# Optimization experiments

Hardware: AMD Instinct MI355X
Metric: run time of the kernel (lower is better)

Reference implementation:

```python
import jax, jax.numpy as jnp
import numpy as np

N_NODES = 100000
N_EDGES = 1600000
IN_FEAT = 128
HIDDEN = 64
OUT_FEAT = 32


def gcn_conv(x, src, dst, W, b, num_nodes):
    """PyG GCNConv: add self-loops, symmetric deg^-1/2 normalization,
    linear transform, scatter-sum aggregation at destination nodes."""
    loops = jnp.arange(num_nodes, dtype=src.dtype)
    s = jnp.concatenate([src, loops])  # [E+N]
    d = jnp.concatenate([dst, loops])  # [E+N]
    deg = jax.ops.segment_sum(jnp.ones_like(d, dtype=x.dtype), d,
                              num_segments=num_nodes)  # in-degree incl. self-loop
    dinv = jnp.where(deg > 0, jax.lax.rsqrt(deg), 0.0)
    norm = dinv[s] * dinv[d]                       # [E+N]
    h = x @ W.T                                    # [N, out] dense GEMM first (PyG order)
    msg = h[s] * norm[:, None]                     # gather + scale, [E+N, out]
    out = jax.ops.segment_sum(msg, d, num_segments=num_nodes)
    return out + b


def setup_inputs() -> dict:
    key = jax.random.key(0)
    k1, k2, k3, k4, k5, k6, k7 = jax.random.split(key, 7)
    x = jax.random.normal(k1, (N_NODES, IN_FEAT), dtype=jnp.float32)
    edge_index = jax.random.randint(k2, (2, N_EDGES), 0, N_NODES, dtype=jnp.int64)
    # Glorot-ish init for linear weights (PyG Linear), zeros bias
    W1 = jax.random.normal(k3, (HIDDEN, IN_FEAT), dtype=jnp.float32) * (1.0 / np.sqrt(IN_FEAT))
    b1 = jnp.zeros((HIDDEN,), dtype=jnp.float32)
    W2 = jax.random.normal(k4, (OUT_FEAT, HIDDEN), dtype=jnp.float32) * (1.0 / np.sqrt(HIDDEN))
    b2 = jnp.zeros((OUT_FEAT,), dtype=jnp.float32)
    return {"x": x, "edge_index": edge_index, "W1": W1, "b1": b1, "W2": W2, "b2": b2}


def reference(x, edge_index, W1, b1, W2, b2):
    src, dst = edge_index[0], edge_index[1]
    h = gcn_conv(x, src, dst, W1, b1, N_NODES)
    h = jax.nn.relu(h)
    # dropout is identity in eval mode (training=False)
    out = gcn_conv(h, src, dst, W2, b2, N_NODES)
    return out
```

## Files before the change

### kernel.cpp

```cpp
#include <hip/hip_runtime.h>
#include <hip/hip_bf16.h>

#define N_NODES 100000
#define N_EDGES 1600000
#define IN_FEAT 128
#define HIDDEN 64
#define OUT_FEAT 32
#define CAP 64
#define NP 100352
#define PS 68
#define PW 36
#define NBINS 256
#define BIN_NODES 391
#define BIN_CAP 8192
#define EB 4096
#define NBB 391

__device__ __forceinline__ float b2f(unsigned short v) {
    union { unsigned int u; float f; } x;
    x.u = ((unsigned int)v) << 16;
    return x.f;
}
__device__ __forceinline__ unsigned short f2b(float f) {
    union { float f; unsigned int u; } x;
    x.f = f;
    unsigned int r = x.u + 0x7FFFu + ((x.u >> 16) & 1u);
    return (unsigned short)(r >> 16);
}


__global__ __launch_bounds__(256) void k_fused0(const int* __restrict__ src,
                                                const int* __restrict__ dst,
                                                int* __restrict__ binc,
                                                int* __restrict__ ebuf,
                                                const float* __restrict__ x,
                                                const float* __restrict__ W,
                                                unsigned short* __restrict__ u,
                                                int n_edges, int n_nodes) {
    __shared__ float wt[IN_FEAT * HIDDEN];
    int t = threadIdx.x;

    if (blockIdx.x < NBB) {
        int* hist  = (int*)wt;
        int* sbase = (int*)wt + 256;
        hist[t] = 0;
        __syncthreads();

        int estart = blockIdx.x * EB + t * 16;
        int rec[16], bn[16], rk[16];
#pragma unroll
        for (int r = 0; r < 4; ++r) {
            int e = estart + 4 * r;
            if (e + 3 < n_edges) {
                int4 d4 = *(const int4*)(dst + e);
                int4 s4 = *(const int4*)(src + e);
                int dd[4] = {d4.x, d4.y, d4.z, d4.w};
                int ss[4] = {s4.x, s4.y, s4.z, s4.w};
#pragma unroll
                for (int c = 0; c < 4; ++c) {
                    int b = dd[c] / BIN_NODES;
                    bn[4 * r + c] = b;
                    rec[4 * r + c] = ss[c] | ((dd[c] - b * BIN_NODES) << 17);
                }
            } else {
#pragma unroll
                for (int c = 0; c < 4; ++c) {
                    int ee = e + c;
                    bool ok = ee < n_edges;
                    int dd = ok ? dst[ee] : 0;
                    int ss = ok ? src[ee] : 0;
                    int b = dd / BIN_NODES;
                    bn[4 * r + c] = ok ? b : -1;
                    rec[4 * r + c] = ss | ((dd - b * BIN_NODES) << 17);
                }
            }
        }
#pragma unroll
        for (int r = 0; r < 16; ++r)
            rk[r] = (bn[r] >= 0) ? atomicAdd(&hist[bn[r]], 1) : 0;
        __syncthreads();
        sbase[t] = (hist[t] > 0) ? atomicAdd(&binc[t], hist[t]) : 0;
        __syncthreads();
#pragma unroll
        for (int r = 0; r < 16; ++r) {
            if (bn[r] >= 0) {
                int pos = sbase[bn[r]] + rk[r];
                if (pos < BIN_CAP)
                    ebuf[(size_t)bn[r] * BIN_CAP + pos] = rec[r];
            }
        }
        return;
    }

    int bid = blockIdx.x - NBB;
    {
        int k4 = t & 31;
        int f0 = t >> 5;
#pragma unroll
        for (int r = 0; r < 8; ++r) {
            int f = f0 + 8 * r;
            float4 wv = *(const float4*)(W + (size_t)f * IN_FEAT + 4 * k4);
            int g = (f >> 2) ^ (k4 & 15);
            int bse = 4 * g + (f & 3);
            wt[(4 * k4 + 0) * HIDDEN + bse] = wv.x;
            wt[(4 * k4 + 1) * HIDDEN + bse] = wv.y;
            wt[(4 * k4 + 2) * HIDDEN + bse] = wv.z;
            wt[(4 * k4 + 3) * HIDDEN + bse] = wv.w;
        }
    }
    __syncthreads();

    int fi = t & 15;
    int ng = t >> 4;
    int node0 = bid * 64 + 4 * ng;

    const float4* xr[4];
#pragma unroll
    for (int m = 0; m < 4; ++m) {
        int nm = node0 + m;
        if (nm > n_nodes - 1) nm = n_nodes - 1;
        xr[m] = (const float4*)(x + (size_t)nm * IN_FEAT);
    }

    float4 acc[4];
#pragma unroll
    for (int m = 0; m < 4; ++m) acc[m] = make_float4(0.f, 0.f, 0.f, 0.f);

#pragma unroll 8
    for (int k4 = 0; k4 < IN_FEAT / 4; ++k4) {
        float4 xv0 = xr[0][k4];
        float4 xv1 = xr[1][k4];
        float4 xv2 = xr[2][k4];
        float4 xv3 = xr[3][k4];
        const float* wp = wt + (4 * k4) * HIDDEN + 4 * (fi ^ (k4 & 15));
        float4 wv0 = *(const float4*)(wp);
        float4 wv1 = *(const float4*)(wp + HIDDEN);
        float4 wv2 = *(const float4*)(wp + 2 * HIDDEN);
        float4 wv3 = *(const float4*)(wp + 3 * HIDDEN);
#define FMA4(A, XV)                                                        \
        A.x += XV.x * wv0.x + XV.y * wv1.x + XV.z * wv2.x + XV.w * wv3.x;  \
        A.y += XV.x * wv0.y + XV.y * wv1.y + XV.z * wv2.y + XV.w * wv3.y;  \
        A.z += XV.x * wv0.z + XV.y * wv1.z + XV.z * wv2.z + XV.w * wv3.z;  \
        A.w += XV.x * wv0.w + XV.y * wv1.w + XV.z * wv2.w + XV.w * wv3.w;
        FMA4(acc[0], xv0)
        FMA4(acc[1], xv1)
        FMA4(acc[2], xv2)
        FMA4(acc[3], xv3)
#undef FMA4
    }

#pragma unroll
    for (int m = 0; m < 4; ++m) {
        int node = node0 + m;
        if (node < n_nodes) {
            ushort4 o;
            o.x = f2b(acc[m].x); o.y = f2b(acc[m].y);
            o.z = f2b(acc[m].z); o.w = f2b(acc[m].w);
            *(ushort4*)(u + (size_t)node * HIDDEN + 4 * fi) = o;
        }
    }
}


__global__ __launch_bounds__(256) void k_binB(const int* __restrict__ binc,
                                              const int* __restrict__ ebuf,
                                              int* __restrict__ csr,
                                              int* __restrict__ deg,
                                              unsigned short* __restrict__ u,
                                              unsigned short* __restrict__ h2,
                                              int n_nodes) {
    __shared__ int lcur[BIN_NODES];
    int t = threadIdx.x;
    int b = blockIdx.x;

    for (int i = t; i < BIN_NODES; i += 256) lcur[i] = 0;
    __syncthreads();

    int cnt = binc[b];
    if (cnt > BIN_CAP) cnt = BIN_CAP;
    const int* eb = ebuf + (size_t)b * BIN_CAP;
    int nbase = b * BIN_NODES;

    for (int i = t; i < cnt; i += 256) {
        int v = eb[i];
        int sv = v & 0x1FFFF;
        int dl = v >> 17;
        int p = atomicAdd(&lcur[dl], 1);
        if (p < CAP) csr[(size_t)(nbase + dl) * CAP + p] = sv;
    }
    __syncthreads();

    for (int i = t; i < BIN_NODES; i += 256) {
        int node = nbase + i;
        if (node < n_nodes) {
            int dg = lcur[i];
            deg[node] = dg;
            int dgc = dg > CAP ? CAP : dg;
            int dgp = (dgc + 7) & ~7;
            for (int p = dgc; p < dgp; ++p)
                csr[(size_t)node * CAP + p] = n_nodes;
        }
    }
    for (int i = t; i < BIN_NODES * 16; i += 256) {
        int nl = i >> 4;
        int node = nbase + nl;
        if (node < n_nodes) {
            float dv = rsqrtf((float)(lcur[nl] + 1));
            ushort4* p = (ushort4*)(u + (size_t)node * HIDDEN) + (i & 15);
            ushort4 v = *p;
            v.x = f2b(b2f(v.x) * dv);
            v.y = f2b(b2f(v.y) * dv);
            v.z = f2b(b2f(v.z) * dv);
            v.w = f2b(b2f(v.w) * dv);
            *p = v;
        }
    }
    if (b == 0) {
        ushort4 z; z.x = z.y = z.z = z.w = 0;
        if (t < 16) ((ushort4*)(u + (size_t)n_nodes * HIDDEN))[t] = z;
        if (t < 8)  ((ushort4*)(h2 + (size_t)n_nodes * OUT_FEAT))[t] = z;
    }
}


__global__ __launch_bounds__(256) void k_aggg(const unsigned short* __restrict__ u,
                                              const int* __restrict__ degA,
                                              const int* __restrict__ csr,
                                              const float* __restrict__ b1,
                                              const float* __restrict__ W2,
                                              unsigned short* __restrict__ h2,
                                              int n_nodes) {
    __shared__ int   sidx[16 * PS];
    __shared__ float sa[16 * PS];
    __shared__ float sdv[16];
    __shared__ float wt2[HIDDEN * PW];

    int t = threadIdx.x;
    int node0 = blockIdx.x * 16;

    for (int idx = t; idx < OUT_FEAT * HIDDEN; idx += 256) {
        int f = idx >> 6, k = idx & 63;
        wt2[k * PW + f] = W2[idx];
    }
    {
        int nl = t >> 4, pos = t & 15;
        int4 c = *(const int4*)(csr + (size_t)(node0 + nl) * CAP + 4 * pos);
        *(int4*)(sidx + nl * PS + 4 * pos) = c;
    }
    __syncthreads();

    int g = t >> 4;
    int l = t & 15;
    int node = node0 + g;
    int dg = degA[node];
    float dv = rsqrtf((float)(dg + 1));
    if (l == 0) sdv[g] = dv;
    int dgc = dg > CAP ? CAP : dg;
    int dgp = (dgc + 7) & ~7;

    ushort4 sv4 = *(const ushort4*)(u + (size_t)node * HIDDEN + 4 * l);
    float4 acc = make_float4(b2f(sv4.x), b2f(sv4.y), b2f(sv4.z), b2f(sv4.w));
    const int* row = sidx + g * PS;
    for (int j = 0; j < dgp; j += 8) {
        int s0 = row[j],     s1 = row[j + 1], s2 = row[j + 2], s3 = row[j + 3];
        int s4 = row[j + 4], s5 = row[j + 5], s6 = row[j + 6], s7 = row[j + 7];
        ushort4 r0 = *(const ushort4*)(u + (size_t)s0 * HIDDEN + 4 * l);
        ushort4 r1 = *(const ushort4*)(u + (size_t)s1 * HIDDEN + 4 * l);
        ushort4 r2 = *(const ushort4*)(u + (size_t)s2 * HIDDEN + 4 * l);
        ushort4 r3 = *(const ushort4*)(u + (size_t)s3 * HIDDEN + 4 * l);
        ushort4 r4 = *(const ushort4*)(u + (size_t)s4 * HIDDEN + 4 * l);
        ushort4 r5 = *(const ushort4*)(u + (size_t)s5 * HIDDEN + 4 * l);
        ushort4 r6 = *(const ushort4*)(u + (size_t)s6 * HIDDEN + 4 * l);
        ushort4 r7 = *(const ushort4*)(u + (size_t)s7 * HIDDEN + 4 * l);
        acc.x += ((b2f(r0.x) + b2f(r1.x)) + (b2f(r2.x) + b2f(r3.x)))
               + ((b2f(r4.x) + b2f(r5.x)) + (b2f(r6.x) + b2f(r7.x)));
        acc.y += ((b2f(r0.y) + b2f(r1.y)) + (b2f(r2.y) + b2f(r3.y)))
               + ((b2f(r4.y) + b2f(r5.y)) + (b2f(r6.y) + b2f(r7.y)));
        acc.z += ((b2f(r0.z) + b2f(r1.z)) + (b2f(r2.z) + b2f(r3.z)))
               + ((b2f(r4.z) + b2f(r5.z)) + (b2f(r6.z) + b2f(r7.z)));
        acc.w += ((b2f(r0.w) + b2f(r1.w)) + (b2f(r2.w) + b2f(r3.w)))
               + ((b2f(r4.w) + b2f(r5.w)) + (b2f(r6.w) + b2f(r7.w)));
    }

    float4 b1v = *(const float4*)(b1 + 4 * l);
    float4 a;
    a.x = fmaxf(acc.x * dv + b1v.x, 0.f);
    a.y = fmaxf(acc.y * dv + b1v.y, 0.f);
    a.z = fmaxf(acc.z * dv + b1v.z, 0.f);
    a.w = fmaxf(acc.w * dv + b1v.w, 0.f);
    *(float4*)(sa + g * PS + 4 * l) = a;
    __syncthreads();

    int nl = t >> 4;
    int fi = (t >> 1) & 7;
    int dup = t & 1;
    const float* ap = sa + nl * PS + dup * 32;
    const float* wp = wt2 + (dup * 32) * PW + 4 * fi;
    float4 p = make_float4(0.f, 0.f, 0.f, 0.f);
#pragma unroll
    for (int k = 0; k < 32; ++k) {
        float av = ap[k];
        float4 wv = *(const float4*)(wp + k * PW);
        p.x += av * wv.x; p.y += av * wv.y;
        p.z += av * wv.z; p.w += av * wv.w;
    }
    p.x += __shfl_xor(p.x, 1);
    p.y += __shfl_xor(p.y, 1);
    p.z += __shfl_xor(p.z, 1);
    p.w += __shfl_xor(p.w, 1);
    if (dup == 0) {
        float dvn = sdv[nl];
        ushort4 o;
        o.x = f2b(p.x * dvn); o.y = f2b(p.y * dvn);
        o.z = f2b(p.z * dvn); o.w = f2b(p.w * dvn);
        *(ushort4*)(h2 + (size_t)(node0 + nl) * OUT_FEAT + 4 * fi) = o;
    }
}


__global__ __launch_bounds__(256) void k_agg32(const unsigned short* __restrict__ h2,
                                               const int* __restrict__ degA,
                                               const int* __restrict__ csr,
                                               const float* __restrict__ b2,
                                               float* __restrict__ out, int n_nodes) {
    __shared__ int sidx[32 * PS];
    int t = threadIdx.x;
    int node0 = blockIdx.x * 32;

#pragma unroll
    for (int r = 0; r < 2; ++r) {
        int i = t + 256 * r;
        int nl = i >> 4, pos = i & 15;
        int4 c = *(const int4*)(csr + (size_t)(node0 + nl) * CAP + 4 * pos);
        *(int4*)(sidx + nl * PS + 4 * pos) = c;
    }
    __syncthreads();

    int g = t >> 3;
    int l = t & 7;
    int node = node0 + g;
    int dg = degA[node];
    float dv = rsqrtf((float)(dg + 1));
    int dgc = dg > CAP ? CAP : dg;
    int dgp = (dgc + 7) & ~7;

    ushort4 sv4 = *(const ushort4*)(h2 + (size_t)node * OUT_FEAT + 4 * l);
    float4 acc = make_float4(b2f(sv4.x), b2f(sv4.y), b2f(sv4.z), b2f(sv4.w));
    const int* row = sidx + g * PS;
    for (int j = 0; j < dgp; j += 8) {
        int s0 = row[j],     s1 = row[j + 1], s2 = row[j + 2], s3 = row[j + 3];
        int s4 = row[j + 4], s5 = row[j + 5], s6 = row[j + 6], s7 = row[j + 7];
        ushort4 r0 = *(const ushort4*)(h2 + (size_t)s0 * OUT_FEAT + 4 * l);
        ushort4 r1 = *(const ushort4*)(h2 + (size_t)s1 * OUT_FEAT + 4 * l);
        ushort4 r2 = *(const ushort4*)(h2 + (size_t)s2 * OUT_FEAT + 4 * l);
        ushort4 r3 = *(const ushort4*)(h2 + (size_t)s3 * OUT_FEAT + 4 * l);
        ushort4 r4 = *(const ushort4*)(h2 + (size_t)s4 * OUT_FEAT + 4 * l);
        ushort4 r5 = *(const ushort4*)(h2 + (size_t)s5 * OUT_FEAT + 4 * l);
        ushort4 r6 = *(const ushort4*)(h2 + (size_t)s6 * OUT_FEAT + 4 * l);
        ushort4 r7 = *(const ushort4*)(h2 + (size_t)s7 * OUT_FEAT + 4 * l);
        acc.x += ((b2f(r0.x) + b2f(r1.x)) + (b2f(r2.x) + b2f(r3.x)))
               + ((b2f(r4.x) + b2f(r5.x)) + (b2f(r6.x) + b2f(r7.x)));
        acc.y += ((b2f(r0.y) + b2f(r1.y)) + (b2f(r2.y) + b2f(r3.y)))
               + ((b2f(r4.y) + b2f(r5.y)) + (b2f(r6.y) + b2f(r7.y)));
        acc.z += ((b2f(r0.z) + b2f(r1.z)) + (b2f(r2.z) + b2f(r3.z)))
               + ((b2f(r4.z) + b2f(r5.z)) + (b2f(r6.z) + b2f(r7.z)));
        acc.w += ((b2f(r0.w) + b2f(r1.w)) + (b2f(r2.w) + b2f(r3.w)))
               + ((b2f(r4.w) + b2f(r5.w)) + (b2f(r6.w) + b2f(r7.w)));
    }
    float4 bv = *(const float4*)(b2 + 4 * l);
    float4 o = make_float4(acc.x * dv + bv.x, acc.y * dv + bv.y,
                           acc.z * dv + bv.z, acc.w * dv + bv.w);
    *(float4*)(out + (size_t)node * OUT_FEAT + 4 * l) = o;
}

extern "C" void kernel_launch(void* const* d_in, const int* in_sizes, int n_in,
                              void* d_out, int out_size, void* d_ws, size_t ws_size,
                              hipStream_t stream) {
    const float* x  = (const float*)d_in[0];
    const int* ei   = (const int*)d_in[1];
    const float* W1 = (const float*)d_in[2];
    const float* b1 = (const float*)d_in[3];
    const float* W2 = (const float*)d_in[4];
    const float* b2 = (const float*)d_in[5];
    float* out = (float*)d_out;

    const int* src = ei;
    const int* dst = ei + N_EDGES;

    int* deg  = (int*)d_ws;
    int* binc = deg + NP;
    int* csr  = binc + 512;
    int* ebuf = csr + (size_t)N_NODES * CAP;
    unsigned short* u  = (unsigned short*)(ebuf + (size_t)NBINS * BIN_CAP);
    unsigned short* h2 = u + (size_t)(N_NODES + 1) * HIDDEN;

    hipMemsetAsync(binc, 0, 512 * sizeof(int), stream);

    k_fused0<<<NBB + 1563, 256, 0, stream>>>(src, dst, binc, ebuf, x, W1, u,
                                             N_EDGES, N_NODES);

    k_binB<<<NBINS, 256, 0, stream>>>(binc, ebuf, csr, deg, u, h2, N_NODES);

    k_aggg<<<N_NODES / 16, 256, 0, stream>>>(u, deg, csr, b1, W2, h2, N_NODES);

    k_agg32<<<N_NODES / 32, 256, 0, stream>>>(h2, deg, csr, b2, out, N_NODES);
}
```

Before: 228.8 us.

## Stage x tiles into LDS with async global_load_lds double buffering in GEMM

The GEMM part of the fused first kernel now streams x rows into shared memory using direct global-to-LDS loads, in four double-buffered chunks of 32 features per node. Compute reads x from LDS instead of issuing per-thread strided global loads. The goal is coalesced x loads that overlap with the FMA work. In exchange, shared memory grows from 32KB to 48KB per block, which may reduce occupancy, and there are extra barriers per chunk.

```diff
diff --git a/kernel.cpp b/kernel.cpp
--- a/kernel.cpp
+++ b/kernel.cpp
@@ -28,6 +28,12 @@
     return (unsigned short)(r >> 16);
 }
 
+__device__ __forceinline__ void gl_lds16(const float* g, void* l) {
+    __builtin_amdgcn_global_load_lds(
+        (const __attribute__((address_space(1))) void*)g,
+        (__attribute__((address_space(3))) void*)l, 16, 0, 0);
+}
+
 
 __global__ __launch_bounds__(256) void k_fused0(const int* __restrict__ src,
                                                 const int* __restrict__ dst,
@@ -37,12 +43,12 @@
                                                 const float* __restrict__ W,
                                                 unsigned short* __restrict__ u,
                                                 int n_edges, int n_nodes) {
-    __shared__ float wt[IN_FEAT * HIDDEN];
+    __shared__ __align__(16) unsigned char smraw[49152];
     int t = threadIdx.x;
 
     if (blockIdx.x < NBB) {
-        int* hist  = (int*)wt;
-        int* sbase = (int*)wt + 256;
+        int* hist  = (int*)smraw;
+        int* sbase = (int*)smraw + 256;
         hist[t] = 0;
         __syncthreads();
 
@@ -93,6 +99,9 @@
     }
 
     int bid = blockIdx.x - NBB;
+    float*  wt = (float*)smraw;
+    float4* xb = (float4*)(smraw + 32768);
+
     {
         int k4 = t & 31;
         int f0 = t >> 5;
@@ -108,50 +117,62 @@
             wt[(4 * k4 + 3) * HIDDEN + bse] = wv.w;
         }
     }
-    __syncthreads();
+
+    int node0 = bid * 64;
+    int snode = t & 63;
+    int k4a = t >> 6;
+    int nclamp = node0 + snode;
+    if (nclamp > n_nodes - 1) nclamp = n_nodes - 1;
+    const float* grow = x + (size_t)nclamp * IN_FEAT + 4 * k4a;
+    int slot0 = k4a * 64 + snode;
+
+    gl_lds16(grow,      xb + slot0);
+    gl_lds16(grow + 16, xb + slot0 + 256);
 
     int fi = t & 15;
     int ng = t >> 4;
-    int node0 = bid * 64 + 4 * ng;
-
-    const float4* xr[4];
+
+    float4 acc[4];
+#pragma unroll
+    for (int m = 0; m < 4; ++m) acc[m] = make_float4(0.f, 0.f, 0.f, 0.f);
+
+    for (int c = 0; c < 4; ++c) {
+        __syncthreads();
+        if (c < 3) {
+            const float* gnext = grow + (c + 1) * 32;
+            float4* dbuf = xb + ((c + 1) & 1) * 512;
+            gl_lds16(gnext,      dbuf + slot0);
+            gl_lds16(gnext + 16, dbuf + slot0 + 256);
+        }
+        const float4* xc = xb + (c & 1) * 512 + 4 * ng;
+#pragma unroll
+        for (int k4 = 0; k4 < 8; ++k4) {
+            int kg = c * 8 + k4;
+            float4 xv0 = xc[k4 * 64 + 0];
+            float4 xv1 = xc[k4 * 64 + 1];
+            float4 xv2 = xc[k4 * 64 + 2];
+            float4 xv3 = xc[k4 * 64 + 3];
+            const float* wp = wt + (4 * kg) * HIDDEN + 4 * (fi ^ (kg & 15));
+            float4 wv0 = *(const float4*)(wp);
+            float4 wv1 = *(const float4*)(wp + HIDDEN);
+            float4 wv2 = *(const float4*)(wp + 2 * HIDDEN);
+            float4 wv3 = *(const float4*)(wp + 3 * HIDDEN);
+#define FMA4(A, XV)                                                        \
+            A.x += XV.x * wv0.x + XV.y * wv1.x + XV.z * wv2.x + XV.w * wv3.x;  \
+            A.y += XV.x * wv0.y + XV.y * wv1.y + XV.z * wv2.y + XV.w * wv3.y;  \
+            A.z += XV.x * wv0.z + XV.y * wv1.z + XV.z * wv2.z + XV.w * wv3.z;  \
+            A.w += XV.x * wv0.w + XV.y * wv1.w + XV.z * wv2.w + XV.w * wv3.w;
+            FMA4(acc[0], xv0)
+            FMA4(acc[1], xv1)
+            FMA4(acc[2], xv2)
+            FMA4(acc[3], xv3)
+#undef FMA4
+        }
+    }
+
 #pragma unroll
     for (int m = 0; m < 4; ++m) {
-        int nm = node0 + m;
-        if (nm > n_nodes - 1) nm = n_nodes - 1;
-        xr[m] = (const float4*)(x + (size_t)nm * IN_FEAT);
-    }
-
-    float4 acc[4];
-#pragma unroll
-    for (int m = 0; m < 4; ++m) acc[m] = make_float4(0.f, 0.f, 0.f, 0.f);
-
-#pragma unroll 8
-    for (int k4 = 0; k4 < IN_FEAT / 4; ++k4) {
-        float4 xv0 = xr[0][k4];
-        float4 xv1 = xr[1][k4];
-        float4 xv2 = xr[2][k4];
-        float4 xv3 = xr[3][k4];
-        const float* wp = wt + (4 * k4) * HIDDEN + 4 * (fi ^ (k4 & 15));
-        float4 wv0 = *(const float4*)(wp);
-        float4 wv1 = *(const float4*)(wp + HIDDEN);
-        float4 wv2 = *(const float4*)(wp + 2 * HIDDEN);
-        float4 wv3 = *(const float4*)(wp + 3 * HIDDEN);
-#define FMA4(A, XV)                                                        \
-        A.x += XV.x * wv0.x + XV.y * wv1.x + XV.z * wv2.x + XV.w * wv3.x;  \
-        A.y += XV.x * wv0.y + XV.y * wv1.y + XV.z * wv2.y + XV.w * wv3.y;  \
-        A.z += XV.x * wv0.z + XV.y * wv1.z + XV.z * wv2.z + XV.w * wv3.z;  \
-        A.w += XV.x * wv0.w + XV.y * wv1.w + XV.z * wv2.w + XV.w * wv3.w;
-        FMA4(acc[0], xv0)
-        FMA4(acc[1], xv1)
-        FMA4(acc[2], xv2)
-        FMA4(acc[3], xv3)
-#undef FMA4
-    }
-
-#pragma unroll
-    for (int m = 0; m < 4; ++m) {
-        int node = node0 + m;
+        int node = node0 + 4 * ng + m;
         if (node < n_nodes) {
             ushort4 o;
             o.x = f2b(acc[m].x); o.y = f2b(acc[m].y);
```

After: 220.0 us. 3.8% less time.

## Restructure first-layer GEMM to one node per thread with async LDS x staging

Applied to the files above, without the earlier changes.

The dense x@W1 part of the fused kernel is rewritten so each thread computes all 64 outputs for one node, with 256 nodes per block and 391 GEMM blocks instead of 1563. Rows of x are streamed into LDS with double-buffered global_load_lds copies, and W1 is read through wave-uniform (scalar-cacheable) global loads instead of a transposed, swizzled LDS copy. The goal is to cut LDS weight traffic and overlap x loading with compute. In exchange each thread holds 64 accumulators, which raises register pressure and may lower occupancy; W1 reads also now depend on cache hits.

```diff
diff --git a/kernel.cpp b/kernel.cpp
--- a/kernel.cpp
+++ b/kernel.cpp
@@ -15,6 +15,7 @@
 #define BIN_CAP 8192
 #define EB 4096
 #define NBB 391
+#define GEMM_BLKS 391
 
 __device__ __forceinline__ float b2f(unsigned short v) {
     union { unsigned int u; float f; } x;
@@ -26,6 +27,12 @@
     x.f = f;
     unsigned int r = x.u + 0x7FFFu + ((x.u >> 16) & 1u);
     return (unsigned short)(r >> 16);
+}
+
+__device__ __forceinline__ void gl_lds16(const float* g, void* l) {
+    __builtin_amdgcn_global_load_lds(
+        (const __attribute__((address_space(1))) void*)g,
+        (__attribute__((address_space(3))) void*)l, 16, 0, 0);
 }
 
 
@@ -37,12 +44,12 @@
                                                 const float* __restrict__ W,
                                                 unsigned short* __restrict__ u,
                                                 int n_edges, int n_nodes) {
-    __shared__ float wt[IN_FEAT * HIDDEN];
+    __shared__ __align__(16) unsigned char smraw[32768];
     int t = threadIdx.x;
 
     if (blockIdx.x < NBB) {
-        int* hist  = (int*)wt;
-        int* sbase = (int*)wt + 256;
+        int* hist  = (int*)smraw;
+        int* sbase = (int*)smraw + 256;
         hist[t] = 0;
         __syncthreads();
 
@@ -93,70 +100,63 @@
     }
 
     int bid = blockIdx.x - NBB;
-    {
-        int k4 = t & 31;
-        int f0 = t >> 5;
-#pragma unroll
-        for (int r = 0; r < 8; ++r) {
-            int f = f0 + 8 * r;
-            float4 wv = *(const float4*)(W + (size_t)f * IN_FEAT + 4 * k4);
-            int g = (f >> 2) ^ (k4 & 15);
-            int bse = 4 * g + (f & 3);
-            wt[(4 * k4 + 0) * HIDDEN + bse] = wv.x;
-            wt[(4 * k4 + 1) * HIDDEN + bse] = wv.y;
-            wt[(4 * k4 + 2) * HIDDEN + bse] = wv.z;
-            wt[(4 * k4 + 3) * HIDDEN + bse] = wv.w;
-        }
-    }
-    __syncthreads();
-
-    int fi = t & 15;
-    int ng = t >> 4;
-    int node0 = bid * 64 + 4 * ng;
-
-    const float4* xr[4];
-#pragma unroll
-    for (int m = 0; m < 4; ++m) {
-        int nm = node0 + m;
-        if (nm > n_nodes - 1) nm = n_nodes - 1;
-        xr[m] = (const float4*)(x + (size_t)nm * IN_FEAT);
-    }
-
-    float4 acc[4];
-#pragma unroll
-    for (int m = 0; m < 4; ++m) acc[m] = make_float4(0.f, 0.f, 0.f, 0.f);
-
-#pragma unroll 8
-    for (int k4 = 0; k4 < IN_FEAT / 4; ++k4) {
-        float4 xv0 = xr[0][k4];
-        float4 xv1 = xr[1][k4];
-        float4 xv2 = xr[2][k4];
-        float4 xv3 = xr[3][k4];
-        const float* wp = wt + (4 * k4) * HIDDEN + 4 * (fi ^ (k4 & 15));
-        float4 wv0 = *(const float4*)(wp);
-        float4 wv1 = *(const float4*)(wp + HIDDEN);
-        float4 wv2 = *(const float4*)(wp + 2 * HIDDEN);
-        float4 wv3 = *(const float4*)(wp + 3 * HIDDEN);
-#define FMA4(A, XV)                                                        \
-        A.x += XV.x * wv0.x + XV.y * wv1.x + XV.z * wv2.x + XV.w * wv3.x;  \
-        A.y += XV.x * wv0.y + XV.y * wv1.y + XV.z * wv2.y + XV.w * wv3.y;  \
-        A.z += XV.x * wv0.z + XV.y * wv1.z + XV.z * wv2.z + XV.w * wv3.z;  \
-        A.w += XV.x * wv0.w + XV.y * wv1.w + XV.z * wv2.w + XV.w * wv3.w;
-        FMA4(acc[0], xv0)
-        FMA4(acc[1], xv1)
-        FMA4(acc[2], xv2)
-        FMA4(acc[3], xv3)
-#undef FMA4
-    }
-
-#pragma unroll
-    for (int m = 0; m < 4; ++m) {
-        int node = node0 + m;
-        if (node < n_nodes) {
-            ushort4 o;
-            o.x = f2b(acc[m].x); o.y = f2b(acc[m].y);
-            o.z = f2b(acc[m].z); o.w = f2b(acc[m].w);
-            *(ushort4*)(u + (size_t)node * HIDDEN + 4 * fi) = o;
+    float4* xb = (float4*)smraw;
+    int lane = t & 63;
+    int w = t >> 6;
+    int node0 = bid * 256;
+    int mynode = node0 + t;
+
+    const float* gsrc[4];
+#pragma unroll
+    for (int s = 0; s < 4; ++s) {
+        int n = node0 + s * 64 + lane;
+        if (n > n_nodes - 1) n = n_nodes - 1;
+        gsrc[s] = x + (size_t)n * IN_FEAT + 4 * w;
+    }
+    int dslot = w * 256 + lane;
+
+#pragma unroll
+    for (int s = 0; s < 4; ++s)
+        gl_lds16(gsrc[s], xb + dslot + s * 64);
+
+    float acc[64];
+#pragma unroll
+    for (int f = 0; f < 64; ++f) acc[f] = 0.f;
+
+    for (int c = 0; c < 8; ++c) {
+        __syncthreads();
+        if (c < 7) {
+            float4* db = xb + ((c + 1) & 1) * 1024;
+#pragma unroll
+            for (int s = 0; s < 4; ++s)
+                gl_lds16(gsrc[s] + (c + 1) * 16, db + dslot + s * 64);
+        }
+        const float4* xc = xb + (c & 1) * 1024 + t;
+        const float* wbase = W + c * 16;
+#pragma unroll
+        for (int q = 0; q < 4; ++q) {
+            float4 xv = xc[q * 256];
+#pragma unroll
+            for (int f = 0; f < 64; ++f) {
+                float4 wv = *(const float4*)(wbase + (size_t)f * IN_FEAT + 4 * q);
+                acc[f] = fmaf(xv.w, wv.w,
+                          fmaf(xv.z, wv.z,
+                           fmaf(xv.y, wv.y,
+                            fmaf(xv.x, wv.x, acc[f]))));
+            }
+        }
+    }
+
+    if (mynode < n_nodes) {
+        unsigned int* urow = (unsigned int*)(u + (size_t)mynode * HIDDEN);
+#pragma unroll
+        for (int i = 0; i < 8; ++i) {
+            uint4 o;
+            o.x = (unsigned)f2b(acc[8 * i + 0]) | ((unsigned)f2b(acc[8 * i + 1]) << 16);
+            o.y = (unsigned)f2b(acc[8 * i + 2]) | ((unsigned)f2b(acc[8 * i + 3]) << 16);
+            o.z = (unsigned)f2b(acc[8 * i + 4]) | ((unsigned)f2b(acc[8 * i + 5]) << 16);
+            o.w = (unsigned)f2b(acc[8 * i + 6]) | ((unsigned)f2b(acc[8 * i + 7]) << 16);
+            *((uint4*)urow + i) = o;
         }
     }
 }
@@ -396,8 +396,8 @@
 
     hipMemsetAsync(binc, 0, 512 * sizeof(int), stream);
 
-    k_fused0<<<NBB + 1563, 256, 0, stream>>>(src, dst, binc, ebuf, x, W1, u,
-                                             N_EDGES, N_NODES);
+    k_fused0<<<NBB + GEMM_BLKS, 256, 0, stream>>>(src, dst, binc, ebuf, x, W1, u,
+                                                  N_EDGES, N_NODES);
 
     k_binB<<<NBINS, 256, 0, stream>>>(binc, ebuf, csr, deg, u, h2, N_NODES);
 
```

After: 278.8 us. +21.9%, slower.
